# Kernel tuning notes

Hardware: AMD Instinct MI355X
Metric: run time of the kernel (lower is better)

Reference implementation:

```python
import jax, jax.numpy as jnp
import numpy as np

D_MODEL = 512
N_LAYERS = 4
VOCAB = 256
SEQ = 2048
BATCH = 8
EPS = 1e-5


def _ln(x, g, b):
    mu = jnp.mean(x, axis=-1, keepdims=True)
    var = jnp.mean(jnp.square(x - mu), axis=-1, keepdims=True)
    return (x - mu) * jax.lax.rsqrt(var + EPS) * g + b


def setup_inputs() -> dict:
    key = jax.random.key(0)
    ks = jax.random.split(key, 16)
    d, dff = D_MODEL, 4 * D_MODEL
    s = 0.02
    inp = {
        "tokens": jax.random.randint(ks[0], (BATCH, SEQ), 0, VOCAB, dtype=jnp.int64),
        "emb": jax.random.normal(ks[1], (VOCAB, d), jnp.float32) * s,
        "W_upd": jax.random.normal(ks[2], (d, d), jnp.float32) * s,
        "b_upd": jnp.zeros((d,), jnp.float32),
        "W_f": jax.random.normal(ks[3], (d, d), jnp.float32) * s,
        "b_f": jnp.zeros((d,), jnp.float32),
        "decay_param": jnp.zeros((1,), jnp.float32),
        "norm_g": jnp.ones((d,), jnp.float32),
        "norm_b": jnp.zeros((d,), jnp.float32),
        "cms_ln_g": jnp.ones((N_LAYERS, d), jnp.float32),
        "cms_ln_b": jnp.zeros((N_LAYERS, d), jnp.float32),
        "cms_W1": jax.random.normal(ks[4], (N_LAYERS, d, dff), jnp.float32) * s,
        "cms_b1": jnp.zeros((N_LAYERS, dff), jnp.float32),
        "cms_W2": jax.random.normal(ks[5], (N_LAYERS, dff, d), jnp.float32) * s,
        "cms_b2": jnp.zeros((N_LAYERS, d), jnp.float32),
        "head_W": jax.random.normal(ks[6], (d, VOCAB), jnp.float32) * s,
        "head_b": jnp.zeros((VOCAB,), jnp.float32),
    }
    return inp


def _fast_memory(x, mask, W_upd, b_upd, W_f, b_f, decay_param):
    # x: (B,S,d), mask: (B,S) float
    decay = jax.nn.sigmoid(decay_param[0])
    u = jnp.einsum("bsd,de->bse", x, W_upd) + b_upd  # precompute updates
    u_t = jnp.swapaxes(u, 0, 1)                        # (S,B,d)
    m_t = jnp.swapaxes(mask, 0, 1)[..., None]          # (S,B,1)

    def step(mem, inp):
        u_i, msk = inp
        new = decay * mem + u_i
        mem = msk * new + (1.0 - msk) * mem
        return mem, mem

    mem0 = jnp.zeros((x.shape[0], x.shape[2]), x.dtype)
    _, mems = jax.lax.scan(step, mem0, (u_t, m_t))     # (S,B,d)
    mems = jnp.swapaxes(mems, 0, 1)                    # (B,S,d)
    return jnp.einsum("bsd,de->bse", mems, W_f) + b_f


def reference(tokens, emb, W_upd, b_upd, W_f, b_f, decay_param, norm_g, norm_b,
              cms_ln_g, cms_ln_b, cms_W1, cms_b1, cms_W2, cms_b2, head_W, head_b):
    mask = (tokens != 0).astype(emb.dtype)
    x = emb[tokens]                                    # (B,S,d)
    x = x + _fast_memory(x, mask, W_upd, b_upd, W_f, b_f, decay_param)
    x = _ln(x, norm_g, norm_b)
    for i in range(N_LAYERS):
        h = _ln(x, cms_ln_g[i], cms_ln_b[i])
        h = jax.nn.gelu(jnp.einsum("bsd,df->bsf", h, cms_W1[i]) + cms_b1[i], approximate=False)
        h = jnp.einsum("bsf,fd->bsd", h, cms_W2[i]) + cms_b2[i]
        x = x + h
    return jnp.einsum("bsd,dv->bsv", x, head_W) + head_b
```

## Files before the change

kernel.cpp:

```cpp
#include <hip/hip_runtime.h>
#include <hip/hip_bf16.h>
#include <math.h>

#define D_MODEL 512
#define N_LAYERS 4
#define SEQ 2048
#define BATCH 8
#define M_TOT (BATCH * SEQ)
#define DFF 2048
#define HEAD_V 256
#define SC 32
#define NC (SEQ / SC)

typedef __hip_bfloat16 bf16;
typedef __bf16 bf16x8 __attribute__((ext_vector_type(8)));
typedef float f32x4 __attribute__((ext_vector_type(4)));

__device__ __forceinline__ unsigned short bfbits(float x) {
    bf16 h = __float2bfloat16(x);
    return *(unsigned short*)&h;
}
__device__ __forceinline__ unsigned int pk(float a, float b) {
    return (unsigned int)bfbits(a) | ((unsigned int)bfbits(b) << 16);
}

__device__ __forceinline__ float gelu_f(float x) {
    float t2 = 1.5957691216f * (x + 0.044715f * x * x * x);
    float e = __expf(t2);
    return x - x * __builtin_amdgcn_rcpf(e + 1.0f);
}

__global__ void convT_kernel(const float* __restrict__ W, bf16* __restrict__ WT,
                             int R, int C, size_t wstride, size_t tstride) {
    W += (size_t)blockIdx.z * wstride;
    WT += (size_t)blockIdx.z * tstride;
    __shared__ float t[32][33];
    int r0 = blockIdx.x * 32, c0 = blockIdx.y * 32;
    int tx = threadIdx.x, ty = threadIdx.y;
    #pragma unroll
    for (int i = 0; i < 32; i += 8)
        t[ty + i][tx] = W[(size_t)(r0 + ty + i) * C + c0 + tx];
    __syncthreads();
    #pragma unroll
    for (int i = 0; i < 32; i += 8)
        WT[(size_t)(c0 + ty + i) * R + r0 + tx] = __float2bfloat16(t[tx][ty + i]);
}

__global__ void embed_kernel(const int* __restrict__ tokens,
                             const float* __restrict__ emb,
                             float* __restrict__ xf, bf16* __restrict__ xb) {
    int row = blockIdx.x, t = threadIdx.x;
    int tok = tokens[row];
    float4 v = ((const float4*)(emb + (size_t)tok * D_MODEL))[t];
    ((float4*)(xf + (size_t)row * D_MODEL))[t] = v;
    uint2 st; st.x = pk(v.x, v.y); st.y = pk(v.z, v.w);
    ((uint2*)(xb + (size_t)row * D_MODEL))[t] = st;
}

__global__ void scanA_kernel(bf16* __restrict__ u, const int* __restrict__ tokens,
                             const float* __restrict__ decayp,
                             float* __restrict__ L, float* __restrict__ P) {
    int idx = blockIdx.x;
    int dblk = idx & 1;
    int c = (idx >> 1) & (NC - 1);
    int b = idx >> 7;
    int d = dblk * 256 + threadIdx.x;
    float decay = 1.0f / (1.0f + __expf(-decayp[0]));
    const int* tok = tokens + (size_t)b * SEQ + c * SC;
    bf16* up = u + ((size_t)b * SEQ + (size_t)c * SC) * D_MODEL + d;
    float mem = 0.0f;
    #pragma unroll 4
    for (int s = 0; s < SC; ++s) {
        float ui = __bfloat162float(up[(size_t)s * D_MODEL]);
        bool m = (tok[s] != 0);
        mem = (m ? decay : 1.0f) * mem + (m ? ui : 0.0f);
        up[(size_t)s * D_MODEL] = __float2bfloat16(mem);
    }
    L[((size_t)b * NC + c) * D_MODEL + d] = mem;
    if (threadIdx.x == 0 && dblk == 0) {
        int cnt = 0;
        for (int s = 0; s < SC; ++s) cnt += (tok[s] != 0);
        P[b * NC + c] = __powf(decay, (float)cnt);
    }
}

__global__ void scanB_kernel(const float* __restrict__ L, const float* __restrict__ P,
                             float* __restrict__ Mc) {
    int b = blockIdx.x >> 1;
    int d = (blockIdx.x & 1) * 256 + threadIdx.x;
    float carry = 0.0f;
    for (int c = 0; c < NC; ++c) {
        size_t off = ((size_t)b * NC + c) * D_MODEL + d;
        Mc[off] = carry;
        carry = P[b * NC + c] * carry + L[off];
    }
}

__global__ void scanC_kernel(bf16* __restrict__ u, const int* __restrict__ tokens,
                             const float* __restrict__ decayp,
                             const float* __restrict__ Mc) {
    int idx = blockIdx.x;
    int dblk = idx & 1;
    int c = (idx >> 1) & (NC - 1);
    int b = idx >> 7;
    if (c == 0) return;
    int d = dblk * 256 + threadIdx.x;
    float decay = 1.0f / (1.0f + __expf(-decayp[0]));
    const int* tok = tokens + (size_t)b * SEQ + c * SC;
    bf16* up = u + ((size_t)b * SEQ + (size_t)c * SC) * D_MODEL + d;
    float carry = Mc[((size_t)b * NC + c) * D_MODEL + d];
    float coeff = 1.0f;
    #pragma unroll 4
    for (int s = 0; s < SC; ++s) {
        bool m = (tok[s] != 0);
        coeff *= (m ? decay : 1.0f);
        float local = __bfloat162float(up[(size_t)s * D_MODEL]);
        up[(size_t)s * D_MODEL] = __float2bfloat16(local + carry * coeff);
    }
}

__device__ __forceinline__ void ln_body(const float* __restrict__ in,
                                        float* __restrict__ outf,
                                        bf16* __restrict__ outb,
                                        const float* __restrict__ g,
                                        const float* __restrict__ b,
                                        int WF, int WB) {
    int w = threadIdx.x >> 6, lane = threadIdx.x & 63;
    int row = blockIdx.x * 4 + w;
    const float4* ip = (const float4*)(in + (size_t)row * D_MODEL);
    float4 v0 = ip[lane * 2], v1 = ip[lane * 2 + 1];
    float s1 = v0.x + v0.y + v0.z + v0.w + v1.x + v1.y + v1.z + v1.w;
    float s2 = v0.x * v0.x + v0.y * v0.y + v0.z * v0.z + v0.w * v0.w +
               v1.x * v1.x + v1.y * v1.y + v1.z * v1.z + v1.w * v1.w;
    #pragma unroll
    for (int off = 32; off; off >>= 1) {
        s1 += __shfl_xor(s1, off);
        s2 += __shfl_xor(s2, off);
    }
    float mu = s1 * (1.0f / D_MODEL);
    float var = s2 * (1.0f / D_MODEL) - mu * mu;
    float rstd = rsqrtf(var + 1e-5f);
    const float4* g4 = (const float4*)g;
    const float4* b4 = (const float4*)b;
    float4 g0 = g4[lane * 2], g1 = g4[lane * 2 + 1];
    float4 b0 = b4[lane * 2], b1 = b4[lane * 2 + 1];
    float4 o0, o1;
    o0.x = (v0.x - mu) * rstd * g0.x + b0.x;
    o0.y = (v0.y - mu) * rstd * g0.y + b0.y;
    o0.z = (v0.z - mu) * rstd * g0.z + b0.z;
    o0.w = (v0.w - mu) * rstd * g0.w + b0.w;
    o1.x = (v1.x - mu) * rstd * g1.x + b1.x;
    o1.y = (v1.y - mu) * rstd * g1.y + b1.y;
    o1.z = (v1.z - mu) * rstd * g1.z + b1.z;
    o1.w = (v1.w - mu) * rstd * g1.w + b1.w;
    if (WF) {
        float4* op = (float4*)(outf + (size_t)row * D_MODEL);
        op[lane * 2] = o0; op[lane * 2 + 1] = o1;
    }
    if (WB) {
        uint4 st;
        st.x = pk(o0.x, o0.y); st.y = pk(o0.z, o0.w);
        st.z = pk(o1.x, o1.y); st.w = pk(o1.z, o1.w);
        ((uint4*)(outb + (size_t)row * D_MODEL))[lane] = st;
    }
}

__global__ void ln_f32_kernel(const float* __restrict__ in, float* __restrict__ outf,
                              const float* __restrict__ g, const float* __restrict__ b) {
    ln_body(in, outf, nullptr, g, b, 1, 0);
}
__global__ void ln_b16_kernel(const float* __restrict__ in, bf16* __restrict__ outb,
                              const float* __restrict__ g, const float* __restrict__ b) {
    ln_body(in, nullptr, outb, g, b, 0, 1);
}

#define STAGE(buf, k0)                                                        \
    do {                                                                      \
        _Pragma("unroll")                                                     \
        for (int it = 0; it < AL; ++it) {                                     \
            int cc = tid + it * 512;                                          \
            int rr = cc >> 3, ss = cc & 7;                                    \
            __builtin_amdgcn_global_load_lds(                                 \
                A + (size_t)(m0 + rr) * K + (k0) + 8 * (ss ^ (rr & 7)),       \
                smem + (buf) * TILEB + cc * 16, 16, 0, 0);                    \
        }                                                                     \
        _Pragma("unroll")                                                     \
        for (int it = 0; it < 4; ++it) {                                      \
            int cc = tid + it * 512;                                          \
            int rr = cc >> 3, ss = cc & 7;                                    \
            __builtin_amdgcn_global_load_lds(                                 \
                BT + (size_t)(n0 + rr) * K + (k0) + 8 * (ss ^ (rr & 7)),      \
                smem + (buf) * TILEB + BM * 128 + cc * 16, 16, 0, 0);         \
        }                                                                     \
    } while (0)

template <int WM, int GELU, int RES, int OBF>
__device__ __forceinline__ void gemm_body(char* smem,
                          const bf16* __restrict__ A, const bf16* __restrict__ BT,
                          const float* __restrict__ bias, const float* __restrict__ R,
                          float* __restrict__ Cf, bf16* __restrict__ Cb,
                          int N, int K) {
    constexpr int BM = 2 * WM;
    constexpr int MI = WM / 16;
    constexpr int AL = BM / 64;
    constexpr int TILEB = (BM + 256) * 128;
    constexpr int ST = 68;
    const int tid = threadIdx.x;
    const int lane = tid & 63;
    const int w = tid >> 6;
    const int wr = w >> 2, wc = w & 3;
    const int lm = lane & 15, lk = lane >> 4;
    const int swz = (lm & 7) << 4;
    const int m0 = blockIdx.x * BM, n0 = blockIdx.y * 256;

    f32x4 acc[MI][4] = {};
    const int nt = K >> 6;

    STAGE(0, 0);
    int cur = 0;
    for (int t = 0; t < nt; ++t) {
        if (t + 1 < nt) {
            STAGE(cur ^ 1, (t + 1) * 64);
            if constexpr (AL == 4) asm volatile("s_waitcnt vmcnt(8)" ::: "memory");
            else                   asm volatile("s_waitcnt vmcnt(6)" ::: "memory");
        } else {
            asm volatile("s_waitcnt vmcnt(0)" ::: "memory");
        }
        __builtin_amdgcn_s_barrier();
        __builtin_amdgcn_sched_barrier(0);
        const char* Ab = smem + cur * TILEB;
        const char* Bb = Ab + BM * 128;
        #pragma unroll
        for (int ks = 0; ks < 2; ++ks) {
            bf16x8 fb[4];
            #pragma unroll
            for (int nf = 0; nf < 4; ++nf)
                fb[nf] = *(const bf16x8*)(Bb + (wc * 64 + nf * 16 + lm) * 128 +
                                          ((ks * 64 + lk * 16) ^ swz));
            #pragma unroll
            for (int mh = 0; mh < MI / 4; ++mh) {
                bf16x8 fa[4];
                #pragma unroll
                for (int mf = 0; mf < 4; ++mf)
                    fa[mf] = *(const bf16x8*)(Ab + (wr * WM + (mh * 4 + mf) * 16 + lm) * 128 +
                                              ((ks * 64 + lk * 16) ^ swz));
                __builtin_amdgcn_s_setprio(1);
                #pragma unroll
                for (int mf = 0; mf < 4; ++mf)
                    #pragma unroll
                    for (int nf = 0; nf < 4; ++nf)
                        acc[mh * 4 + mf][nf] = __builtin_amdgcn_mfma_f32_16x16x32_bf16(
                            fa[mf], fb[nf], acc[mh * 4 + mf][nf], 0, 0, 0);
                __builtin_amdgcn_s_setprio(0);
            }
        }
        __builtin_amdgcn_s_barrier();
        cur ^= 1;
    }
    __syncthreads();

    float* ep = (float*)smem + w * 16 * ST;
    const int r2 = lane >> 2;
    const int q = lane & 3;
    const int gc0 = n0 + wc * 64 + q * 16;
    #pragma unroll
    for (int i = 0; i < MI; ++i) {
        #pragma unroll
        for (int nf = 0; nf < 4; ++nf)
            #pragma unroll
            for (int r = 0; r < 4; ++r)
                ep[(lk * 4 + r) * ST + nf * 16 + lm] = acc[i][nf][r];
        int grow = m0 + wr * WM + i * 16 + r2;
        float4 fx[4];
        #pragma unroll
        for (int v = 0; v < 4; ++v)
            fx[v] = *(const float4*)&ep[r2 * ST + q * 16 + v * 4];
        #pragma unroll
        for (int v = 0; v < 4; ++v) {
            float4 bb = *(const float4*)(bias + gc0 + v * 4);
            fx[v].x += bb.x; fx[v].y += bb.y; fx[v].z += bb.z; fx[v].w += bb.w;
            if (GELU) {
                fx[v].x = gelu_f(fx[v].x);
                fx[v].y = gelu_f(fx[v].y);
                fx[v].z = gelu_f(fx[v].z);
                fx[v].w = gelu_f(fx[v].w);
            }
            if (RES) {
                float4 rr = *(const float4*)(R + (size_t)grow * N + gc0 + v * 4);
                fx[v].x += rr.x; fx[v].y += rr.y; fx[v].z += rr.z; fx[v].w += rr.w;
            }
        }
        if (OBF == 0 || OBF == 2) {
            #pragma unroll
            for (int v = 0; v < 4; ++v)
                *(float4*)(Cf + (size_t)grow * N + gc0 + v * 4) = fx[v];
        }
        if (OBF >= 1) {
            uint4 s1, s2;
            s1.x = pk(fx[0].x, fx[0].y); s1.y = pk(fx[0].z, fx[0].w);
            s1.z = pk(fx[1].x, fx[1].y); s1.w = pk(fx[1].z, fx[1].w);
            s2.x = pk(fx[2].x, fx[2].y); s2.y = pk(fx[2].z, fx[2].w);
            s2.z = pk(fx[3].x, fx[3].y); s2.w = pk(fx[3].z, fx[3].w);
            *(uint4*)(Cb + (size_t)grow * N + gc0) = s1;
            *(uint4*)(Cb + (size_t)grow * N + gc0 + 8) = s2;
        }
    }
}

#define DEF_GEMM(name, WM, GELU, RES, OBF)                                    \
__launch_bounds__(512) __global__ void name(                                  \
        const bf16* __restrict__ A, const bf16* __restrict__ BT,              \
        const float* __restrict__ bias, const float* __restrict__ R,          \
        float* __restrict__ Cf, bf16* __restrict__ Cb, int N, int K) {        \
    __shared__ char smem[2 * ((2 * (WM)) + 256) * 128];                       \
    gemm_body<WM, GELU, RES, OBF>(smem, A, BT, bias, R, Cf, Cb, N, K);        \
}

DEF_GEMM(gemm_gelu,    128, 1, 0, 1)
DEF_GEMM(gemm_u,        64, 0, 0, 1)
DEF_GEMM(gemm_res,      64, 0, 1, 0)
DEF_GEMM(gemm_resboth,  64, 0, 1, 2)
DEF_GEMM(gemm_plain,    64, 0, 0, 0)

extern "C" void kernel_launch(void* const* d_in, const int* in_sizes, int n_in,
                              void* d_out, int out_size, void* d_ws, size_t ws_size,
                              hipStream_t stream) {
    const int*   tokens = (const int*)d_in[0];
    const float* emb    = (const float*)d_in[1];
    const float* W_upd  = (const float*)d_in[2];
    const float* b_upd  = (const float*)d_in[3];
    const float* W_f    = (const float*)d_in[4];
    const float* b_f    = (const float*)d_in[5];
    const float* decayp = (const float*)d_in[6];
    const float* norm_g = (const float*)d_in[7];
    const float* norm_b = (const float*)d_in[8];
    const float* cms_g  = (const float*)d_in[9];
    const float* cms_b  = (const float*)d_in[10];
    const float* cW1    = (const float*)d_in[11];
    const float* cb1    = (const float*)d_in[12];
    const float* cW2    = (const float*)d_in[13];
    const float* cb2    = (const float*)d_in[14];
    const float* head_W = (const float*)d_in[15];
    const float* head_b = (const float*)d_in[16];
    float* out = (float*)d_out;

    const int M = M_TOT, D = D_MODEL, F = DFF, V = HEAD_V;

    float* xf = (float*)d_ws;
    bf16*  lnb = (bf16*)((char*)d_ws + (size_t)M * D * 4);
    bf16*  wb  = (bf16*)((char*)lnb + (size_t)M * D * 2);
    const size_t WB_ELEMS = 9043968;
    char* dyn = (char*)wb + WB_ELEMS * 2;
    size_t used = (size_t)(dyn - (char*)d_ws);
    size_t avail = ws_size > used ? ws_size - used : 0;
    int MC = 4096;
    if (avail >= (size_t)16384 * F * 2) MC = 16384;
    else if (avail >= (size_t)8192 * F * 2) MC = 8192;
    bf16* ub = (bf16*)dyn;
    bf16* hb = (bf16*)dyn;

    float* scanL = out;
    float* scanM = out + (size_t)BATCH * NC * D;
    float* scanP = scanM + (size_t)BATCH * NC * D;

    bf16* WupdT = wb;
    bf16* WfT   = wb + 262144;
    bf16* W1T   = wb + 524288;
    bf16* W2T   = wb + 4718592;
    bf16* HWT   = wb + 8912896;

    dim3 tb(32, 8);
    convT_kernel<<<dim3(16, 16, 2), tb, 0, stream>>>(W_upd, WupdT, D, D,
                                                     (size_t)(W_f - W_upd), 262144);
    convT_kernel<<<dim3(16, 64, N_LAYERS), tb, 0, stream>>>(cW1, W1T, D, F,
                                                            (size_t)D * F, 1048576);
    convT_kernel<<<dim3(64, 16, N_LAYERS), tb, 0, stream>>>(cW2, W2T, F, D,
                                                            (size_t)F * D, 1048576);
    convT_kernel<<<dim3(16, 8, 1), tb, 0, stream>>>(head_W, HWT, D, V, 0, 0);

    embed_kernel<<<M, 128, 0, stream>>>(tokens, emb, xf, lnb);

    gemm_u<<<dim3(M / 128, D / 256), 512, 0, stream>>>(
        lnb, WupdT, b_upd, nullptr, nullptr, ub, D, D);
    scanA_kernel<<<BATCH * NC * 2, 256, 0, stream>>>(ub, tokens, decayp, scanL, scanP);
    scanB_kernel<<<BATCH * 2, 256, 0, stream>>>(scanL, scanP, scanM);
    scanC_kernel<<<BATCH * NC * 2, 256, 0, stream>>>(ub, tokens, decayp, scanM);
    gemm_res<<<dim3(M / 128, D / 256), 512, 0, stream>>>(
        ub, WfT, b_f, xf, xf, nullptr, D, D);
    ln_f32_kernel<<<M / 4, 256, 0, stream>>>(xf, xf, norm_g, norm_b);

    for (int l = 0; l < N_LAYERS; ++l) {
        ln_b16_kernel<<<M / 4, 256, 0, stream>>>(xf, lnb,
                                                 cms_g + (size_t)l * D,
                                                 cms_b + (size_t)l * D);
        bool last = (l == N_LAYERS - 1);
        for (int mc = 0; mc < M; mc += MC) {
            gemm_gelu<<<dim3(MC / 256, F / 256), 512, 0, stream>>>(
                lnb + (size_t)mc * D, W1T + (size_t)l * 1048576,
                cb1 + (size_t)l * F, nullptr, nullptr, hb, F, D);
            if (last)
                gemm_resboth<<<dim3(MC / 128, D / 256), 512, 0, stream>>>(
                    hb, W2T + (size_t)l * 1048576, cb2 + (size_t)l * D,
                    xf + (size_t)mc * D, xf + (size_t)mc * D,
                    lnb + (size_t)mc * D, D, F);
            else
                gemm_res<<<dim3(MC / 128, D / 256), 512, 0, stream>>>(
                    hb, W2T + (size_t)l * 1048576, cb2 + (size_t)l * D,
                    xf + (size_t)mc * D, xf + (size_t)mc * D, nullptr, D, F);
        }
    }

    gemm_plain<<<dim3(M / 128, V / 256), 512, 0, stream>>>(
        lnb, HWT, head_b, nullptr, out, nullptr, V, D);
}
```

Before: 539.1 us.

## Use triple-buffered LDS pipeline and shrink K-tile for the GELU GEMM

Moves the bf16 MFMA GEMM from double-buffered to triple-buffered global_load_lds staging, so loads are issued two K-tiles ahead. The wait counts are adjusted to match. The 256-row GELU GEMM drops its K tile from 64 to 32 so three buffers fit in LDS, and it gets a new swizzle pattern for the 64-byte rows. The other GEMMs keep BK=64 with three buffers, which raises LDS use and may reduce occupancy.

```diff
diff --git a/kernel.cpp b/kernel.cpp
--- a/kernel.cpp
+++ b/kernel.cpp
@@ -177,73 +177,85 @@
 #define STAGE(buf, k0)                                                        \
     do {                                                                      \
         _Pragma("unroll")                                                     \
-        for (int it = 0; it < AL; ++it) {                                     \
+        for (int it = 0; it < AIT; ++it) {                                    \
             int cc = tid + it * 512;                                          \
-            int rr = cc >> 3, ss = cc & 7;                                    \
+            int l = cc ^ ((cc >> 3) & 7);                                     \
             __builtin_amdgcn_global_load_lds(                                 \
-                A + (size_t)(m0 + rr) * K + (k0) + 8 * (ss ^ (rr & 7)),       \
+                A + (size_t)(m0 + l / CHR) * K + (k0) + (l % CHR) * 8,        \
                 smem + (buf) * TILEB + cc * 16, 16, 0, 0);                    \
         }                                                                     \
         _Pragma("unroll")                                                     \
-        for (int it = 0; it < 4; ++it) {                                      \
+        for (int it = 0; it < BIT; ++it) {                                    \
             int cc = tid + it * 512;                                          \
-            int rr = cc >> 3, ss = cc & 7;                                    \
+            int l = cc ^ ((cc >> 3) & 7);                                     \
             __builtin_amdgcn_global_load_lds(                                 \
-                BT + (size_t)(n0 + rr) * K + (k0) + 8 * (ss ^ (rr & 7)),      \
-                smem + (buf) * TILEB + BM * 128 + cc * 16, 16, 0, 0);         \
+                BT + (size_t)(n0 + l / CHR) * K + (k0) + (l % CHR) * 8,       \
+                smem + (buf) * TILEB + BM * BK * 2 + cc * 16, 16, 0, 0);      \
         }                                                                     \
     } while (0)
 
-template <int WM, int GELU, int RES, int OBF>
+template <int BMODE, int GELU, int RES, int OBF>
 __device__ __forceinline__ void gemm_body(char* smem,
                           const bf16* __restrict__ A, const bf16* __restrict__ BT,
                           const float* __restrict__ bias, const float* __restrict__ R,
                           float* __restrict__ Cf, bf16* __restrict__ Cb,
                           int N, int K) {
-    constexpr int BM = 2 * WM;
+    constexpr int BM = BMODE ? 128 : 256;
+    constexpr int BK = BMODE ? 64 : 32;
+    constexpr int WM = BM / 2;
     constexpr int MI = WM / 16;
-    constexpr int AL = BM / 64;
-    constexpr int TILEB = (BM + 256) * 128;
+    constexpr int KS = BK / 32;
+    constexpr int CHR = BK / 8;
+    constexpr int AIT = BM * BK * 2 / 16 / 512;
+    constexpr int BIT = 256 * BK * 2 / 16 / 512;
+    constexpr int TILEB = (BM + 256) * BK * 2;
     constexpr int ST = 68;
     const int tid = threadIdx.x;
     const int lane = tid & 63;
     const int w = tid >> 6;
     const int wr = w >> 2, wc = w & 3;
     const int lm = lane & 15, lk = lane >> 4;
-    const int swz = (lm & 7) << 4;
+    const int swz = BMODE ? ((lm & 7) << 4) : (((lm >> 1) & 7) << 4);
     const int m0 = blockIdx.x * BM, n0 = blockIdx.y * 256;
 
     f32x4 acc[MI][4] = {};
-    const int nt = K >> 6;
+    const int nt = K / BK;
 
     STAGE(0, 0);
+    STAGE(1, BK);
     int cur = 0;
     for (int t = 0; t < nt; ++t) {
-        if (t + 1 < nt) {
-            STAGE(cur ^ 1, (t + 1) * 64);
-            if constexpr (AL == 4) asm volatile("s_waitcnt vmcnt(8)" ::: "memory");
-            else                   asm volatile("s_waitcnt vmcnt(6)" ::: "memory");
+        if (t + 2 < nt) {
+            int nb = cur + 2; if (nb >= 3) nb -= 3;
+            STAGE(nb, (t + 2) * BK);
+            if constexpr (BMODE == 0) asm volatile("s_waitcnt vmcnt(8)" ::: "memory");
+            else                      asm volatile("s_waitcnt vmcnt(12)" ::: "memory");
+        } else if (t + 1 < nt) {
+            if constexpr (BMODE == 0) asm volatile("s_waitcnt vmcnt(4)" ::: "memory");
+            else                      asm volatile("s_waitcnt vmcnt(6)" ::: "memory");
         } else {
             asm volatile("s_waitcnt vmcnt(0)" ::: "memory");
         }
         __builtin_amdgcn_s_barrier();
         __builtin_amdgcn_sched_barrier(0);
         const char* Ab = smem + cur * TILEB;
-        const char* Bb = Ab + BM * 128;
+        const char* Bb = Ab + BM * BK * 2;
         #pragma unroll
-        for (int ks = 0; ks < 2; ++ks) {
+        for (int ks = 0; ks < KS; ++ks) {
             bf16x8 fb[4];
             #pragma unroll
-            for (int nf = 0; nf < 4; ++nf)
-                fb[nf] = *(const bf16x8*)(Bb + (wc * 64 + nf * 16 + lm) * 128 +
-                                          ((ks * 64 + lk * 16) ^ swz));
+            for (int nf = 0; nf < 4; ++nf) {
+                int boff = (wc * 64 + nf * 16 + lm) * BK * 2 + ks * 64 + lk * 16;
+                fb[nf] = *(const bf16x8*)(Bb + (boff ^ swz));
+            }
             #pragma unroll
             for (int mh = 0; mh < MI / 4; ++mh) {
                 bf16x8 fa[4];
                 #pragma unroll
-                for (int mf = 0; mf < 4; ++mf)
-                    fa[mf] = *(const bf16x8*)(Ab + (wr * WM + (mh * 4 + mf) * 16 + lm) * 128 +
-                                              ((ks * 64 + lk * 16) ^ swz));
+                for (int mf = 0; mf < 4; ++mf) {
+                    int aoff = (wr * WM + (mh * 4 + mf) * 16 + lm) * BK * 2 + ks * 64 + lk * 16;
+                    fa[mf] = *(const bf16x8*)(Ab + (aoff ^ swz));
+                }
                 __builtin_amdgcn_s_setprio(1);
                 #pragma unroll
                 for (int mf = 0; mf < 4; ++mf)
@@ -255,7 +267,7 @@
             }
         }
         __builtin_amdgcn_s_barrier();
-        cur ^= 1;
+        cur = (cur == 2) ? 0 : cur + 1;
     }
     __syncthreads();
 
@@ -307,20 +319,20 @@
     }
 }
 
-#define DEF_GEMM(name, WM, GELU, RES, OBF)                                    \
+#define DEF_GEMM(name, BMODE, GELU, RES, OBF)                                 \
 __launch_bounds__(512) __global__ void name(                                  \
         const bf16* __restrict__ A, const bf16* __restrict__ BT,              \
         const float* __restrict__ bias, const float* __restrict__ R,          \
         float* __restrict__ Cf, bf16* __restrict__ Cb, int N, int K) {        \
-    __shared__ char smem[2 * ((2 * (WM)) + 256) * 128];                       \
-    gemm_body<WM, GELU, RES, OBF>(smem, A, BT, bias, R, Cf, Cb, N, K);        \
-}
-
-DEF_GEMM(gemm_gelu,    128, 1, 0, 1)
-DEF_GEMM(gemm_u,        64, 0, 0, 1)
-DEF_GEMM(gemm_res,      64, 0, 1, 0)
-DEF_GEMM(gemm_resboth,  64, 0, 1, 2)
-DEF_GEMM(gemm_plain,    64, 0, 0, 0)
+    __shared__ char smem[3 * (((BMODE) ? 128 : 256) + 256) * ((BMODE) ? 64 : 32) * 2]; \
+    gemm_body<BMODE, GELU, RES, OBF>(smem, A, BT, bias, R, Cf, Cb, N, K);     \
+}
+
+DEF_GEMM(gemm_gelu,    0, 1, 0, 1)
+DEF_GEMM(gemm_u,       1, 0, 0, 1)
+DEF_GEMM(gemm_res,     1, 0, 1, 0)
+DEF_GEMM(gemm_resboth, 1, 0, 1, 2)
+DEF_GEMM(gemm_plain,   1, 0, 0, 0)
 
 extern "C" void kernel_launch(void* const* d_in, const int* in_sizes, int n_in,
                               void* d_out, int out_size, void* d_ws, size_t ws_size,
```

After: 557.5 us. +3.4%, slower.

## Shrink GEMM K-tile to 32 and unify 128x256 tiles for higher occupancy

Applied to the files above, without the earlier changes.

Every GEMM now uses one 128x256 block tile with a K step of 32 instead of 64. The LDS swizzle is rewritten for 64-byte rows, and the launch bounds request 4 blocks per CU. The gelu GEMM drops from 256-row tiles to 128-row tiles, which doubles its grid. This cuts LDS use per block so more blocks can be resident and latency is hidden through occupancy, at the cost of twice as many barriers and loop iterations per K and less operand reuse in the gelu GEMM.

```diff
diff --git a/kernel.cpp b/kernel.cpp
--- a/kernel.cpp
+++ b/kernel.cpp
@@ -176,84 +176,74 @@
 
 #define STAGE(buf, k0)                                                        \
     do {                                                                      \
-        _Pragma("unroll")                                                     \
-        for (int it = 0; it < AL; ++it) {                                     \
-            int cc = tid + it * 512;                                          \
-            int rr = cc >> 3, ss = cc & 7;                                    \
+        {                                                                     \
+            int cc = tid;                                                     \
+            int l = cc ^ ((cc >> 3) & 7);                                     \
             __builtin_amdgcn_global_load_lds(                                 \
-                A + (size_t)(m0 + rr) * K + (k0) + 8 * (ss ^ (rr & 7)),       \
+                A + (size_t)(m0 + (l >> 2)) * K + (k0) + (l & 3) * 8,         \
                 smem + (buf) * TILEB + cc * 16, 16, 0, 0);                    \
         }                                                                     \
         _Pragma("unroll")                                                     \
-        for (int it = 0; it < 4; ++it) {                                      \
+        for (int it = 0; it < 2; ++it) {                                      \
             int cc = tid + it * 512;                                          \
-            int rr = cc >> 3, ss = cc & 7;                                    \
+            int l = cc ^ ((cc >> 3) & 7);                                     \
             __builtin_amdgcn_global_load_lds(                                 \
-                BT + (size_t)(n0 + rr) * K + (k0) + 8 * (ss ^ (rr & 7)),      \
-                smem + (buf) * TILEB + BM * 128 + cc * 16, 16, 0, 0);         \
+                BT + (size_t)(n0 + (l >> 2)) * K + (k0) + (l & 3) * 8,        \
+                smem + (buf) * TILEB + 8192 + cc * 16, 16, 0, 0);             \
         }                                                                     \
     } while (0)
 
-template <int WM, int GELU, int RES, int OBF>
+template <int GELU, int RES, int OBF>
 __device__ __forceinline__ void gemm_body(char* smem,
                           const bf16* __restrict__ A, const bf16* __restrict__ BT,
                           const float* __restrict__ bias, const float* __restrict__ R,
                           float* __restrict__ Cf, bf16* __restrict__ Cb,
                           int N, int K) {
-    constexpr int BM = 2 * WM;
-    constexpr int MI = WM / 16;
-    constexpr int AL = BM / 64;
-    constexpr int TILEB = (BM + 256) * 128;
+    constexpr int TILEB = (128 + 256) * 64;
     constexpr int ST = 68;
     const int tid = threadIdx.x;
     const int lane = tid & 63;
     const int w = tid >> 6;
     const int wr = w >> 2, wc = w & 3;
     const int lm = lane & 15, lk = lane >> 4;
-    const int swz = (lm & 7) << 4;
-    const int m0 = blockIdx.x * BM, n0 = blockIdx.y * 256;
-
-    f32x4 acc[MI][4] = {};
-    const int nt = K >> 6;
+    const int swz = ((lm >> 1) & 7) << 4;
+    const int m0 = blockIdx.x * 128, n0 = blockIdx.y * 256;
+
+    f32x4 acc[4][4] = {};
+    const int nt = K >> 5;
 
     STAGE(0, 0);
     int cur = 0;
     for (int t = 0; t < nt; ++t) {
         if (t + 1 < nt) {
-            STAGE(cur ^ 1, (t + 1) * 64);
-            if constexpr (AL == 4) asm volatile("s_waitcnt vmcnt(8)" ::: "memory");
-            else                   asm volatile("s_waitcnt vmcnt(6)" ::: "memory");
+            STAGE(cur ^ 1, (t + 1) * 32);
+            asm volatile("s_waitcnt vmcnt(3)" ::: "memory");
         } else {
             asm volatile("s_waitcnt vmcnt(0)" ::: "memory");
         }
         __builtin_amdgcn_s_barrier();
         __builtin_amdgcn_sched_barrier(0);
         const char* Ab = smem + cur * TILEB;
-        const char* Bb = Ab + BM * 128;
-        #pragma unroll
-        for (int ks = 0; ks < 2; ++ks) {
-            bf16x8 fb[4];
+        const char* Bb = Ab + 8192;
+        bf16x8 fa[4], fb[4];
+        #pragma unroll
+        for (int nf = 0; nf < 4; ++nf) {
+            int boff = (wc * 64 + nf * 16 + lm) * 64 + lk * 16;
+            fb[nf] = *(const bf16x8*)(Bb + (boff ^ swz));
+        }
+        #pragma unroll
+        for (int mf = 0; mf < 4; ++mf) {
+            int aoff = (wr * 64 + mf * 16 + lm) * 64 + lk * 16;
+            fa[mf] = *(const bf16x8*)(Ab + (aoff ^ swz));
+        }
+        __builtin_amdgcn_s_setprio(1);
+        #pragma unroll
+        for (int mf = 0; mf < 4; ++mf)
             #pragma unroll
             for (int nf = 0; nf < 4; ++nf)
-                fb[nf] = *(const bf16x8*)(Bb + (wc * 64 + nf * 16 + lm) * 128 +
-                                          ((ks * 64 + lk * 16) ^ swz));
-            #pragma unroll
-            for (int mh = 0; mh < MI / 4; ++mh) {
-                bf16x8 fa[4];
-                #pragma unroll
-                for (int mf = 0; mf < 4; ++mf)
-                    fa[mf] = *(const bf16x8*)(Ab + (wr * WM + (mh * 4 + mf) * 16 + lm) * 128 +
-                                              ((ks * 64 + lk * 16) ^ swz));
-                __builtin_amdgcn_s_setprio(1);
-                #pragma unroll
-                for (int mf = 0; mf < 4; ++mf)
-                    #pragma unroll
-                    for (int nf = 0; nf < 4; ++nf)
-                        acc[mh * 4 + mf][nf] = __builtin_amdgcn_mfma_f32_16x16x32_bf16(
-                            fa[mf], fb[nf], acc[mh * 4 + mf][nf], 0, 0, 0);
-                __builtin_amdgcn_s_setprio(0);
-            }
-        }
+                acc[mf][nf] = __builtin_amdgcn_mfma_f32_16x16x32_bf16(
+                    fa[mf], fb[nf], acc[mf][nf], 0, 0, 0);
+        __builtin_amdgcn_s_setprio(0);
         __builtin_amdgcn_s_barrier();
         cur ^= 1;
     }
@@ -264,13 +254,13 @@
     const int q = lane & 3;
     const int gc0 = n0 + wc * 64 + q * 16;
     #pragma unroll
-    for (int i = 0; i < MI; ++i) {
+    for (int i = 0; i < 4; ++i) {
         #pragma unroll
         for (int nf = 0; nf < 4; ++nf)
             #pragma unroll
             for (int r = 0; r < 4; ++r)
                 ep[(lk * 4 + r) * ST + nf * 16 + lm] = acc[i][nf][r];
-        int grow = m0 + wr * WM + i * 16 + r2;
+        int grow = m0 + wr * 64 + i * 16 + r2;
         float4 fx[4];
         #pragma unroll
         for (int v = 0; v < 4; ++v)
@@ -307,20 +297,20 @@
     }
 }
 
-#define DEF_GEMM(name, WM, GELU, RES, OBF)                                    \
-__launch_bounds__(512) __global__ void name(                                  \
+#define DEF_GEMM(name, GELU, RES, OBF)                                        \
+__launch_bounds__(512, 4) __global__ void name(                               \
         const bf16* __restrict__ A, const bf16* __restrict__ BT,              \
         const float* __restrict__ bias, const float* __restrict__ R,          \
         float* __restrict__ Cf, bf16* __restrict__ Cb, int N, int K) {        \
-    __shared__ char smem[2 * ((2 * (WM)) + 256) * 128];                       \
-    gemm_body<WM, GELU, RES, OBF>(smem, A, BT, bias, R, Cf, Cb, N, K);        \
-}
-
-DEF_GEMM(gemm_gelu,    128, 1, 0, 1)
-DEF_GEMM(gemm_u,        64, 0, 0, 1)
-DEF_GEMM(gemm_res,      64, 0, 1, 0)
-DEF_GEMM(gemm_resboth,  64, 0, 1, 2)
-DEF_GEMM(gemm_plain,    64, 0, 0, 0)
+    __shared__ char smem[2 * (128 + 256) * 64];                               \
+    gemm_body<GELU, RES, OBF>(smem, A, BT, bias, R, Cf, Cb, N, K);            \
+}
+
+DEF_GEMM(gemm_gelu,    1, 0, 1)
+DEF_GEMM(gemm_u,       0, 0, 1)
+DEF_GEMM(gemm_res,     0, 1, 0)
+DEF_GEMM(gemm_resboth, 0, 1, 2)
+DEF_GEMM(gemm_plain,   0, 0, 0)
 
 extern "C" void kernel_launch(void* const* d_in, const int* in_sizes, int n_in,
                               void* d_out, int out_size, void* d_ws, size_t ws_size,
@@ -395,7 +385,7 @@
                                                  cms_b + (size_t)l * D);
         bool last = (l == N_LAYERS - 1);
         for (int mc = 0; mc < M; mc += MC) {
-            gemm_gelu<<<dim3(MC / 256, F / 256), 512, 0, stream>>>(
+            gemm_gelu<<<dim3(MC / 128, F / 256), 512, 0, stream>>>(
                 lnb + (size_t)mc * D, W1T + (size_t)l * 1048576,
                 cb1 + (size_t)l * F, nullptr, nullptr, hb, F, D);
             if (last)
```

After: 568.3 us. +5.4%, slower.
